# Performance work log

Measured on AMD Instinct MI355X. Metric: run time of the kernel, lower is better.

The kernel has to match this reference:

```python
import jax, jax.numpy as jnp
import numpy as np

NB_CAT = 8192       # nb_category per column
RANK = 16           # low-rank factor dimension
N_COLS = 4          # number of categorical columns (len(embedding_sizes))
N_PAIRS = 1048576   # number of (x, y) index pairs
FRAC_DIAG = 0.9     # fraction_diagonal init


def setup_inputs() -> dict:
    key = jax.random.key(0)
    k1, k2, k3, k4 = jax.random.split(key, 4)
    x = jax.random.randint(k1, (N_PAIRS, N_COLS), 0, NB_CAT, dtype=jnp.int32)
    y = jax.random.randint(k2, (N_PAIRS, N_COLS), 0, NB_CAT, dtype=jnp.int32)
    # params initialized as in the torch module, plus small noise so values are non-degenerate
    std = (FRAC_DIAG * jnp.ones((N_COLS, NB_CAT), dtype=jnp.float32)
           + 0.01 * jax.random.normal(k3, (N_COLS, NB_CAT), dtype=jnp.float32))
    covar_factor = ((1.0 - FRAC_DIAG) / np.float32(np.sqrt(RANK))
                    * jnp.ones((N_COLS, NB_CAT, RANK), dtype=jnp.float32)
                    + 0.01 * jax.random.normal(k4, (N_COLS, NB_CAT, RANK), dtype=jnp.float32))
    return {"x": x, "y": y, "covar_factor": covar_factor, "std": std}


def reference(x, y, covar_factor, std):
    # Build full covariance per column: F @ F.T + diag(std^2)   -> [C, N, N]
    cov = jnp.einsum('cnr,cmr->cnm', covar_factor, covar_factor)
    diag_idx = jnp.arange(cov.shape[1])
    cov = cov.at[:, diag_idx, diag_idx].add(std * std)
    # Gather requested (x, y) entries per column, then reduce (should_reduce=True)
    cols = jnp.arange(cov.shape[0])  # [C]
    vals = cov[cols[None, :], x, y]  # [B, C]
    return vals.sum(axis=-1)         # [B]
```

## Files before the change

### kernel.cpp

```cpp
#include <hip/hip_runtime.h>

#define NB_CAT  8192
#define RANK    16
#define N_COLS  4
#define N_PAIRS 1048576

#define NSLICE      16
#define SLICE_ROWS  NB_CAT
#define SLICE_BYTES (SLICE_ROWS * 8)
#define TBL_BYTES   ((size_t)NSLICE * SLICE_BYTES)
#define LDS_BYTES   (2 * SLICE_BYTES)

typedef _Float16 half2_t __attribute__((ext_vector_type(2)));

#if defined(__has_builtin)
#if __has_builtin(__builtin_amdgcn_fdot2)
#define HAVE_FDOT2 1
#endif
#endif

__device__ __forceinline__ float dot4_f16(uint2 A, uint2 B, float acc) {
#ifdef HAVE_FDOT2
    acc = __builtin_amdgcn_fdot2(__builtin_bit_cast(half2_t, A.x), __builtin_bit_cast(half2_t, B.x), acc, false);
    acc = __builtin_amdgcn_fdot2(__builtin_bit_cast(half2_t, A.y), __builtin_bit_cast(half2_t, B.y), acc, false);
#else
    half2_t ax = __builtin_bit_cast(half2_t, A.x), bx = __builtin_bit_cast(half2_t, B.x);
    half2_t ay = __builtin_bit_cast(half2_t, A.y), by = __builtin_bit_cast(half2_t, B.y);
    acc = fmaf((float)ax[0], (float)bx[0], acc); acc = fmaf((float)ax[1], (float)bx[1], acc);
    acc = fmaf((float)ay[0], (float)by[0], acc); acc = fmaf((float)ay[1], (float)by[1], acc);
#endif
    return acc;
}

template <int C> __device__ __forceinline__ int comp(const int4& v) {
    if (C == 0) return v.x;
    if (C == 1) return v.y;
    if (C == 2) return v.z;
    return v.w;
}

__global__ __launch_bounds__(256) void pack_f16_kernel(
    const float4* __restrict__ src, uint2* __restrict__ dst)
{
    const int g = blockIdx.x * 256 + threadIdx.x;
    const int s = g >> 13;
    const int k = g & (NB_CAT - 1);
    const int c = s >> 2, qr = s & 3;

    const float4 f = src[(c * NB_CAT + k) * 4 + qr];
    half2_t p0 = {(_Float16)f.x, (_Float16)f.y};
    half2_t p1 = {(_Float16)f.z, (_Float16)f.w};
    uint2 u;
    u.x = __builtin_bit_cast(unsigned int, p0);
    u.y = __builtin_bit_cast(unsigned int, p1);
    dst[g] = u;
}

__global__ __launch_bounds__(1024, 1) void IndexKernel_32238024524411_kernel(
    const int4*  __restrict__ x4,
    const int4*  __restrict__ y4,
    const uint2* __restrict__ tbl,
    const float* __restrict__ stdv,
    float*       __restrict__ out)
{
    extern __shared__ uint2 sh[];

    const int tid  = threadIdx.x;
    const int base = blockIdx.x * 4096 + tid;

    int4 xv[4], yv[4];
#pragma unroll
    for (int j = 0; j < 4; ++j) {
        xv[j] = x4[base + j * 1024];
        yv[j] = y4[base + j * 1024];
    }

    float acc[4] = {0.f, 0.f, 0.f, 0.f};

    uint2 stg[8];
#pragma unroll
    for (int it = 0; it < 8; ++it) stg[it] = tbl[tid + it * 1024];

#define PHASE(S)                                                               \
    {                                                                          \
        constexpr int s  = (S);                                                \
        constexpr int c  = s >> 2;                                             \
        constexpr int qr = s & 3;                                              \
        uint2* buf = sh + (s & 1) * SLICE_ROWS;                                \
        _Pragma("unroll")                                                      \
        for (int it = 0; it < 8; ++it) buf[tid + it * 1024] = stg[it];         \
        if (s < NSLICE - 1) {                                                  \
            const uint2* nsrc = tbl + (size_t)(s + 1) * SLICE_ROWS;            \
            _Pragma("unroll")                                                  \
            for (int it = 0; it < 8; ++it) stg[it] = nsrc[tid + it * 1024];    \
        }                                                                      \
              \
        asm volatile("s_waitcnt lgkmcnt(0)" ::: "memory");                     \
        __builtin_amdgcn_s_barrier();                                          \
        asm volatile("" ::: "memory");                                         \
        _Pragma("unroll")                                                      \
        for (int j = 0; j < 4; ++j) {                                          \
            const int xi = comp<c>(xv[j]);                                     \
            const int yi = comp<c>(yv[j]);                                     \
            const uint2 a = buf[xi];                                           \
            const uint2 b = buf[yi];                                           \
            acc[j] = dot4_f16(a, b, acc[j]);                                   \
            if (qr == 0 && xi == yi) {                                         \
                const float sd = stdv[c * NB_CAT + xi];                        \
                acc[j] = fmaf(sd, sd, acc[j]);                                 \
            }                                                                  \
        }                                                                      \
        asm volatile("" ::: "memory");                                         \
    }

    PHASE(0)  PHASE(1)  PHASE(2)  PHASE(3)
    PHASE(4)  PHASE(5)  PHASE(6)  PHASE(7)
    PHASE(8)  PHASE(9)  PHASE(10) PHASE(11)
    PHASE(12) PHASE(13) PHASE(14) PHASE(15)
#undef PHASE

#pragma unroll
    for (int j = 0; j < 4; ++j) {
        out[base + j * 1024] = acc[j];
    }
}

__global__ __launch_bounds__(256) void fallback_kernel(
    const int* __restrict__ x, const int* __restrict__ y,
    const float4* __restrict__ cf, const float* __restrict__ stdv,
    float* __restrict__ out)
{
    const int tid = threadIdx.x;
    const int q = tid & 15, gi = tid >> 4, c = q >> 2, s = q & 3;
    const int p0 = blockIdx.x * 32 + gi, p1 = p0 + 16;
    const int rb = c * NB_CAT;
    const int xi0 = x[p0*4+c], yi0 = y[p0*4+c], xi1 = x[p1*4+c], yi1 = y[p1*4+c];
    const float4 a0 = cf[(size_t)(rb+xi0)*4 + s], b0 = cf[(size_t)(rb+yi0)*4 + s];
    const float4 a1 = cf[(size_t)(rb+xi1)*4 + s], b1 = cf[(size_t)(rb+yi1)*4 + s];
    float v0 = a0.x*b0.x; v0 = fmaf(a0.y,b0.y,v0); v0 = fmaf(a0.z,b0.z,v0); v0 = fmaf(a0.w,b0.w,v0);
    float v1 = a1.x*b1.x; v1 = fmaf(a1.y,b1.y,v1); v1 = fmaf(a1.z,b1.z,v1); v1 = fmaf(a1.w,b1.w,v1);
    if (s == 0 && xi0 == yi0) { float sd = stdv[rb+xi0]; v0 = fmaf(sd,sd,v0); }
    if (s == 0 && xi1 == yi1) { float sd = stdv[rb+yi1]; v1 = fmaf(sd,sd,v1); }
    int t;
    t = __builtin_amdgcn_update_dpp(0, __float_as_int(v0), 0xB1, 0xF, 0xF, true); v0 += __int_as_float(t);
    t = __builtin_amdgcn_update_dpp(0, __float_as_int(v0), 0x4E, 0xF, 0xF, true); v0 += __int_as_float(t);
    t = __builtin_amdgcn_update_dpp(0, __float_as_int(v0), 0x141,0xF, 0xF, true); v0 += __int_as_float(t);
    t = __builtin_amdgcn_update_dpp(0, __float_as_int(v0), 0x128,0xF, 0xF, true); v0 += __int_as_float(t);
    t = __builtin_amdgcn_update_dpp(0, __float_as_int(v1), 0xB1, 0xF, 0xF, true); v1 += __int_as_float(t);
    t = __builtin_amdgcn_update_dpp(0, __float_as_int(v1), 0x4E, 0xF, 0xF, true); v1 += __int_as_float(t);
    t = __builtin_amdgcn_update_dpp(0, __float_as_int(v1), 0x141,0xF, 0xF, true); v1 += __int_as_float(t);
    t = __builtin_amdgcn_update_dpp(0, __float_as_int(v1), 0x128,0xF, 0xF, true); v1 += __int_as_float(t);
    if (q == 0) { out[p0] = v0; out[p1] = v1; }
}

extern "C" void kernel_launch(void* const* d_in, const int* in_sizes, int n_in,
                              void* d_out, int out_size, void* d_ws, size_t ws_size,
                              hipStream_t stream) {
    const int*   x    = (const int*)d_in[0];
    const int*   y    = (const int*)d_in[1];
    const float* cf   = (const float*)d_in[2];
    const float* stdv = (const float*)d_in[3];
    float*       out  = (float*)d_out;

    if (ws_size < TBL_BYTES) {
        fallback_kernel<<<N_PAIRS / 32, 256, 0, stream>>>(
            x, y, (const float4*)cf, stdv, out);
        return;
    }

    (void)hipFuncSetAttribute(
        reinterpret_cast<const void*>(&IndexKernel_32238024524411_kernel),
        hipFuncAttributeMaxDynamicSharedMemorySize, LDS_BYTES);

    pack_f16_kernel<<<NSLICE * NB_CAT / 256, 256, 0, stream>>>(
        (const float4*)cf, (uint2*)d_ws);

    IndexKernel_32238024524411_kernel<<<N_PAIRS / 4096, 1024, LDS_BYTES, stream>>>(
        (const int4*)x, (const int4*)y, (const uint2*)d_ws, stdv, out);
}
```

Measured before the change: 96.99 us.

## Stream table slices into LDS with direct global-to-LDS DMA and hoist std diagonal

Replaces the register-staged copy of each table slice (global to VGPR to LDS) with the global_load_lds builtin, which writes 16-byte chunks straight into the double-buffered LDS slice while the current slice is being consumed. The diagonal std² terms are moved out of the slice loop and added once up front. This is meant to cut VGPR pressure and LDS-store instructions and to overlap slice fetches with compute. In exchange it depends on the compiler and hardware supporting the 16-byte LDS DMA width, and synchronisation now relies on __syncthreads, with no explicit vmcnt wait before the next slice is read.

```diff
diff --git a/kernel.cpp b/kernel.cpp
--- a/kernel.cpp
+++ b/kernel.cpp
@@ -16,6 +16,9 @@
 #if defined(__has_builtin)
 #if __has_builtin(__builtin_amdgcn_fdot2)
 #define HAVE_FDOT2 1
+#endif
+#if __has_builtin(__builtin_amdgcn_global_load_lds)
+#define HAVE_DMA 1
 #endif
 #endif
 
@@ -32,12 +35,18 @@
     return acc;
 }
 
-template <int C> __device__ __forceinline__ int comp(const int4& v) {
-    if (C == 0) return v.x;
-    if (C == 1) return v.y;
-    if (C == 2) return v.z;
-    return v.w;
-}
+__device__ __forceinline__ int comp4(const int4& v, int c) {
+    return (c == 0) ? v.x : (c == 1) ? v.y : (c == 2) ? v.z : v.w;
+}
+
+#ifdef HAVE_DMA
+__device__ __forceinline__ void dma16(const void* g, void* l) {
+    __builtin_amdgcn_global_load_lds(
+        (const __attribute__((address_space(1))) void*)g,
+        (__attribute__((address_space(3))) void*)l,
+        16, 0, 0);
+}
+#endif
 
 __global__ __launch_bounds__(256) void pack_f16_kernel(
     const float4* __restrict__ src, uint2* __restrict__ dst)
@@ -77,47 +86,71 @@
 
     float acc[4] = {0.f, 0.f, 0.f, 0.f};
 
+#pragma unroll
+    for (int j = 0; j < 4; ++j) {
+        const int4 a = xv[j], b = yv[j];
+        if (a.x == b.x) { const float s = stdv[0 * NB_CAT + a.x]; acc[j] = fmaf(s, s, acc[j]); }
+        if (a.y == b.y) { const float s = stdv[1 * NB_CAT + a.y]; acc[j] = fmaf(s, s, acc[j]); }
+        if (a.z == b.z) { const float s = stdv[2 * NB_CAT + a.z]; acc[j] = fmaf(s, s, acc[j]); }
+        if (a.w == b.w) { const float s = stdv[3 * NB_CAT + a.w]; acc[j] = fmaf(s, s, acc[j]); }
+    }
+
+#ifdef HAVE_DMA
+#pragma unroll
+    for (int it = 0; it < 4; ++it) {
+        const size_t off = (size_t)(tid + it * 1024) * 16;
+        dma16((const char*)tbl + off, (char*)sh + off);
+    }
+    __syncthreads();
+
+#pragma unroll
+    for (int s = 0; s < NSLICE; ++s) {
+        const int c = s >> 2;
+        if (s < NSLICE - 1) {
+            const char* gsrc = (const char*)(tbl + (size_t)(s + 1) * SLICE_ROWS);
+            char*       ldst = (char*)(sh + ((s + 1) & 1) * SLICE_ROWS);
+#pragma unroll
+            for (int it = 0; it < 4; ++it) {
+                const size_t off = (size_t)(tid + it * 1024) * 16;
+                dma16(gsrc + off, ldst + off);
+            }
+        }
+        const uint2* buf = sh + (s & 1) * SLICE_ROWS;
+#pragma unroll
+        for (int j = 0; j < 4; ++j) {
+            const int xi = comp4(xv[j], c);
+            const int yi = comp4(yv[j], c);
+            const uint2 a = buf[xi];
+            const uint2 b = buf[yi];
+            acc[j] = dot4_f16(a, b, acc[j]);
+        }
+        __syncthreads();
+    }
+#else
     uint2 stg[8];
 #pragma unroll
     for (int it = 0; it < 8; ++it) stg[it] = tbl[tid + it * 1024];
-
-#define PHASE(S)                                                               \
-    {                                                                          \
-        constexpr int s  = (S);                                                \
-        constexpr int c  = s >> 2;                                             \
-        constexpr int qr = s & 3;                                              \
-        uint2* buf = sh + (s & 1) * SLICE_ROWS;                                \
-        _Pragma("unroll")                                                      \
-        for (int it = 0; it < 8; ++it) buf[tid + it * 1024] = stg[it];         \
-        if (s < NSLICE - 1) {                                                  \
-            const uint2* nsrc = tbl + (size_t)(s + 1) * SLICE_ROWS;            \
-            _Pragma("unroll")                                                  \
-            for (int it = 0; it < 8; ++it) stg[it] = nsrc[tid + it * 1024];    \
-        }                                                                      \
-              \
-        asm volatile("s_waitcnt lgkmcnt(0)" ::: "memory");                     \
-        __builtin_amdgcn_s_barrier();                                          \
-        asm volatile("" ::: "memory");                                         \
-        _Pragma("unroll")                                                      \
-        for (int j = 0; j < 4; ++j) {                                          \
-            const int xi = comp<c>(xv[j]);                                     \
-            const int yi = comp<c>(yv[j]);                                     \
-            const uint2 a = buf[xi];                                           \
-            const uint2 b = buf[yi];                                           \
-            acc[j] = dot4_f16(a, b, acc[j]);                                   \
-            if (qr == 0 && xi == yi) {                                         \
-                const float sd = stdv[c * NB_CAT + xi];                        \
-                acc[j] = fmaf(sd, sd, acc[j]);                                 \
-            }                                                                  \
-        }                                                                      \
-        asm volatile("" ::: "memory");                                         \
-    }
-
-    PHASE(0)  PHASE(1)  PHASE(2)  PHASE(3)
-    PHASE(4)  PHASE(5)  PHASE(6)  PHASE(7)
-    PHASE(8)  PHASE(9)  PHASE(10) PHASE(11)
-    PHASE(12) PHASE(13) PHASE(14) PHASE(15)
-#undef PHASE
+#pragma unroll
+    for (int s = 0; s < NSLICE; ++s) {
+        const int c = s >> 2;
+        uint2* buf = sh + (s & 1) * SLICE_ROWS;
+#pragma unroll
+        for (int it = 0; it < 8; ++it) buf[tid + it * 1024] = stg[it];
+        if (s < NSLICE - 1) {
+            const uint2* nsrc = tbl + (size_t)(s + 1) * SLICE_ROWS;
+#pragma unroll
+            for (int it = 0; it < 8; ++it) stg[it] = nsrc[tid + it * 1024];
+        }
+        __syncthreads();
+#pragma unroll
+        for (int j = 0; j < 4; ++j) {
+            const int xi = comp4(xv[j], c);
+            const int yi = comp4(yv[j], c);
+            acc[j] = dot4_f16(buf[xi], buf[yi], acc[j]);
+        }
+        __syncthreads();
+    }
+#endif
 
 #pragma unroll
     for (int j = 0; j < 4; ++j) {
```

Measured after the change: 114.3 us. 17.9% more time.

## Split columns into two groups per block and reduce partials in a separate kernel

Applied to the files above, without the earlier changes.

The main kernel now assigns each block one of two column pairs and 8192 pairs, so each block streams only 8 of the 16 table slices into LDS and processes twice as many pairs per slice. Per-block staging of the table is halved relative to the work done. Each group writes partial sums to workspace, and a new reduce kernel adds them, which costs an extra launch and 12 MB of partial-sum traffic. The std diagonal term is also hoisted out of the phase loop.

```diff
diff --git a/kernel.cpp b/kernel.cpp
--- a/kernel.cpp
+++ b/kernel.cpp
@@ -10,6 +10,8 @@
 #define SLICE_BYTES (SLICE_ROWS * 8)
 #define TBL_BYTES   ((size_t)NSLICE * SLICE_BYTES)
 #define LDS_BYTES   (2 * SLICE_BYTES)
+#define PART_BYTES  ((size_t)N_PAIRS * 4)
+#define WS_NEED     (TBL_BYTES + 2 * PART_BYTES)
 
 typedef _Float16 half2_t __attribute__((ext_vector_type(2)));
 
@@ -32,13 +34,6 @@
     return acc;
 }
 
-template <int C> __device__ __forceinline__ int comp(const int4& v) {
-    if (C == 0) return v.x;
-    if (C == 1) return v.y;
-    if (C == 2) return v.z;
-    return v.w;
-}
-
 __global__ __launch_bounds__(256) void pack_f16_kernel(
     const float4* __restrict__ src, uint2* __restrict__ dst)
 {
@@ -57,40 +52,52 @@
 }
 
 __global__ __launch_bounds__(1024, 1) void IndexKernel_32238024524411_kernel(
-    const int4*  __restrict__ x4,
-    const int4*  __restrict__ y4,
+    const int2*  __restrict__ x2,
+    const int2*  __restrict__ y2,
     const uint2* __restrict__ tbl,
     const float* __restrict__ stdv,
-    float*       __restrict__ out)
+    float*       __restrict__ part)
 {
     extern __shared__ uint2 sh[];
 
-    const int tid  = threadIdx.x;
-    const int base = blockIdx.x * 4096 + tid;
+    const int tid   = threadIdx.x;
+    const int g     = blockIdx.x >> 7;
+    const int chunk = blockIdx.x & 127;
+    const int base  = chunk * 8192 + tid;
 
-    int4 xv[4], yv[4];
+    const uint2* gtbl = tbl + (size_t)(g * 8) * SLICE_ROWS;
+
+    int2 xi[8], yi[8];
 #pragma unroll
-    for (int j = 0; j < 4; ++j) {
-        xv[j] = x4[base + j * 1024];
-        yv[j] = y4[base + j * 1024];
+    for (int j = 0; j < 8; ++j) {
+        const size_t p = (size_t)(base + j * 1024);
+        xi[j] = x2[p * 2 + g];
+        yi[j] = y2[p * 2 + g];
     }
 
-    float acc[4] = {0.f, 0.f, 0.f, 0.f};
+    float acc[8] = {0.f, 0.f, 0.f, 0.f, 0.f, 0.f, 0.f, 0.f};
+
+    const float* sd0 = stdv + (size_t)(2 * g) * NB_CAT;
+    const float* sd1 = stdv + (size_t)(2 * g + 1) * NB_CAT;
+#pragma unroll
+    for (int j = 0; j < 8; ++j) {
+        if (xi[j].x == yi[j].x) { const float s = sd0[xi[j].x]; acc[j] = fmaf(s, s, acc[j]); }
+        if (xi[j].y == yi[j].y) { const float s = sd1[xi[j].y]; acc[j] = fmaf(s, s, acc[j]); }
+    }
 
     uint2 stg[8];
 #pragma unroll
-    for (int it = 0; it < 8; ++it) stg[it] = tbl[tid + it * 1024];
+    for (int it = 0; it < 8; ++it) stg[it] = gtbl[tid + it * 1024];
 
 #define PHASE(S)                                                               \
     {                                                                          \
         constexpr int s  = (S);                                                \
-        constexpr int c  = s >> 2;                                             \
-        constexpr int qr = s & 3;                                              \
+        constexpr int cl = s >> 2;                          \
         uint2* buf = sh + (s & 1) * SLICE_ROWS;                                \
         _Pragma("unroll")                                                      \
         for (int it = 0; it < 8; ++it) buf[tid + it * 1024] = stg[it];         \
-        if (s < NSLICE - 1) {                                                  \
-            const uint2* nsrc = tbl + (size_t)(s + 1) * SLICE_ROWS;            \
+        if (s < 7) {                                                           \
+            const uint2* nsrc = gtbl + (size_t)(s + 1) * SLICE_ROWS;           \
             _Pragma("unroll")                                                  \
             for (int it = 0; it < 8; ++it) stg[it] = nsrc[tid + it * 1024];    \
         }                                                                      \
@@ -99,30 +106,33 @@
         __builtin_amdgcn_s_barrier();                                          \
         asm volatile("" ::: "memory");                                         \
         _Pragma("unroll")                                                      \
-        for (int j = 0; j < 4; ++j) {                                          \
-            const int xi = comp<c>(xv[j]);                                     \
-            const int yi = comp<c>(yv[j]);                                     \
-            const uint2 a = buf[xi];                                           \
-            const uint2 b = buf[yi];                                           \
-            acc[j] = dot4_f16(a, b, acc[j]);                                   \
-            if (qr == 0 && xi == yi) {                                         \
-                const float sd = stdv[c * NB_CAT + xi];                        \
-                acc[j] = fmaf(sd, sd, acc[j]);                                 \
-            }                                                                  \
+        for (int j = 0; j < 8; ++j) {                                          \
+            const int a = cl ? xi[j].y : xi[j].x;                              \
+            const int b = cl ? yi[j].y : yi[j].x;                              \
+            acc[j] = dot4_f16(buf[a], buf[b], acc[j]);                         \
         }                                                                      \
         asm volatile("" ::: "memory");                                         \
     }
 
-    PHASE(0)  PHASE(1)  PHASE(2)  PHASE(3)
-    PHASE(4)  PHASE(5)  PHASE(6)  PHASE(7)
-    PHASE(8)  PHASE(9)  PHASE(10) PHASE(11)
-    PHASE(12) PHASE(13) PHASE(14) PHASE(15)
+    PHASE(0) PHASE(1) PHASE(2) PHASE(3)
+    PHASE(4) PHASE(5) PHASE(6) PHASE(7)
 #undef PHASE
 
+    float* my = part + (size_t)g * N_PAIRS;
 #pragma unroll
-    for (int j = 0; j < 4; ++j) {
-        out[base + j * 1024] = acc[j];
+    for (int j = 0; j < 8; ++j) {
+        my[base + j * 1024] = acc[j];
     }
+}
+
+__global__ __launch_bounds__(256) void reduce_kernel(
+    const float4* __restrict__ p0, const float4* __restrict__ p1,
+    float4* __restrict__ out)
+{
+    const int i = blockIdx.x * 256 + threadIdx.x;
+    const float4 a = p0[i];
+    const float4 b = p1[i];
+    out[i] = float4{a.x + b.x, a.y + b.y, a.z + b.z, a.w + b.w};
 }
 
 __global__ __launch_bounds__(256) void fallback_kernel(
@@ -162,7 +172,7 @@
     const float* stdv = (const float*)d_in[3];
     float*       out  = (float*)d_out;
 
-    if (ws_size < TBL_BYTES) {
+    if (ws_size < WS_NEED) {
         fallback_kernel<<<N_PAIRS / 32, 256, 0, stream>>>(
             x, y, (const float4*)cf, stdv, out);
         return;
@@ -172,9 +182,15 @@
         reinterpret_cast<const void*>(&IndexKernel_32238024524411_kernel),
         hipFuncAttributeMaxDynamicSharedMemorySize, LDS_BYTES);
 
+    uint2* tbl   = (uint2*)d_ws;
+    float* part  = (float*)((char*)d_ws + TBL_BYTES);
+
     pack_f16_kernel<<<NSLICE * NB_CAT / 256, 256, 0, stream>>>(
-        (const float4*)cf, (uint2*)d_ws);
+        (const float4*)cf, tbl);
 
-    IndexKernel_32238024524411_kernel<<<N_PAIRS / 4096, 1024, LDS_BYTES, stream>>>(
-        (const int4*)x, (const int4*)y, (const uint2*)d_ws, stdv, out);
+    IndexKernel_32238024524411_kernel<<<256, 1024, LDS_BYTES, stream>>>(
+        (const int2*)x, (const int2*)y, tbl, stdv, part);
+
+    reduce_kernel<<<N_PAIRS / 4 / 256, 256, 0, stream>>>(
+        (const float4*)part, (const float4*)(part + N_PAIRS), (float4*)out);
 }
```

After: 95.89 us. About the same (-1.1%).
